# Optimization experiments

Measured on AMD Instinct MI355X. Metric: run time of the kernel, lower is better.

The kernel has to match this reference:

```python
import jax, jax.numpy as jnp
import numpy as np

BLOCKSIZE = 4096
OUT_FEATURES = 16384
IN_FEATURES = 4096
BATCH, SEQ = 4, 2048


def setup_inputs() -> dict:
    key = jax.random.key(0)
    k_x, k_w, k_a, k_b = jax.random.split(key, 4)
    x = jax.random.normal(k_x, (BATCH, SEQ, IN_FEATURES), dtype=jnp.float32)
    # quantized int8 weight stored as indices into the 256-entry codebook
    weight_q = jax.random.randint(k_w, (OUT_FEATURES, IN_FEATURES), 0, 256, dtype=jnp.int32)
    n_blocks = (OUT_FEATURES * IN_FEATURES) // BLOCKSIZE  # 16384
    absmax = jax.random.uniform(k_a, (n_blocks,), dtype=jnp.float32) + 0.5
    # bitsandbytes dynamic-map code: a sorted table of values in [-1, 1]
    code = jnp.linspace(-1.0, 1.0, 256, dtype=jnp.float32)
    bias = jax.random.normal(k_b, (OUT_FEATURES,), dtype=jnp.float32) * 0.02
    return {"x": x, "weight_q": weight_q, "absmax": absmax, "code": code, "bias": bias}


def dequantize_blockwise(weight_q, absmax, code):
    # codebook lookup then per-block absmax scaling
    flat = code[weight_q.reshape(-1)]                      # [out*in]
    flat = flat.reshape(-1, BLOCKSIZE) * absmax[:, None]   # [n_blocks, blocksize]
    return flat.reshape(weight_q.shape)                    # [out, in]


def reference(x, weight_q, absmax, code, bias):
    w = dequantize_blockwise(weight_q, absmax, code)       # [out, in] fp32
    # F.linear(x, w, bias) = x @ w.T + bias
    return jnp.einsum("bsi,oi->bso", x, w) + bias
```

## Files before the change

kernel.cpp:

```cpp
#include <hip/hip_runtime.h>
#include <hip/hip_bf16.h>
#include <stdint.h>

#define M_TOTAL 8192
#define N_TOTAL 16384
#define K_TOTAL 4096

#define BM 256
#define BN 256
#define BK 64
#define NKT (K_TOTAL / BK)

using f32x4  = __attribute__((ext_vector_type(4))) float;
using bf16x8 = __attribute__((ext_vector_type(8))) short;

#define UNROLL _Pragma("unroll")

__device__ __forceinline__ unsigned short f2bf(float f) {
    union { float f; unsigned u; } v; v.f = f;
    unsigned r = v.u + 0x7fffu + ((v.u >> 16) & 1u);
    return (unsigned short)(r >> 16);
}

__device__ __forceinline__ void gload_lds16(const void* g, void* l) {
    __builtin_amdgcn_global_load_lds(
        (const __attribute__((address_space(1))) unsigned int*)g,
        (__attribute__((address_space(3))) unsigned int*)l,
        16, 0, 0);
}

__global__ void dequant_w_kernel(const int* __restrict__ q,
                                 const float* __restrict__ am,
                                 const float* __restrict__ code,
                                 unsigned short* __restrict__ wb) {
    __shared__ float lc[256];
    if (threadIdx.x < 256) lc[threadIdx.x] = code[threadIdx.x];
    __syncthreads();
    const int total = (N_TOTAL / 4) * K_TOTAL;
    const int stride = gridDim.x * blockDim.x;
    for (int i = blockIdx.x * blockDim.x + threadIdx.x; i < total; i += stride) {
        int4 v = reinterpret_cast<const int4*>(q)[i];
        float a = am[i >> 10];
        ushort4 o;
        o.x = f2bf(lc[v.x & 255] * a);
        o.y = f2bf(lc[v.y & 255] * a);
        o.z = f2bf(lc[v.z & 255] * a);
        o.w = f2bf(lc[v.w & 255] * a);
        reinterpret_cast<ushort4*>(wb)[i] = o;
    }
}

__global__ void cvt_x_kernel(const float* __restrict__ x,
                             unsigned short* __restrict__ xb) {
    const int total = (M_TOTAL * K_TOTAL) / 4;
    const int stride = gridDim.x * blockDim.x;
    for (int i = blockIdx.x * blockDim.x + threadIdx.x; i < total; i += stride) {
        float4 v = reinterpret_cast<const float4*>(x)[i];
        ushort4 o;
        o.x = f2bf(v.x); o.y = f2bf(v.y); o.z = f2bf(v.z); o.w = f2bf(v.w);
        reinterpret_cast<ushort4*>(xb)[i] = o;
    }
}

#define LOAD_AH(DST, BUFI, MH)                                                    \
    UNROLL for (int mf = 0; mf < 4; ++mf)                                         \
        UNROLL for (int ks = 0; ks < 2; ++ks)                                     \
            DST[mf][ks] = *reinterpret_cast<const bf16x8*>(                       \
                &sA[BUFI][((MH)*128 + arow_base + mf*16)*BK +                     \
                          (((ks*4 + rslot_hi) ^ rslot_xor)*8)]);

#define LOAD_BH(DST, BUFI, NH)                                                    \
    UNROLL for (int nf = 0; nf < 2; ++nf)                                         \
        UNROLL for (int ks = 0; ks < 2; ++ks)                                     \
            DST[nf][ks] = *reinterpret_cast<const bf16x8*>(                       \
                &sB[BUFI][((NH)*128 + brow_base + nf*16)*BK +                     \
                          (((ks*4 + rslot_hi) ^ rslot_xor)*8)]);

#define MFMA_Q(MH, NH, AR, BR)                                                    \
    UNROLL for (int mf = 0; mf < 4; ++mf)                                         \
        UNROLL for (int nf = 0; nf < 2; ++nf) {                                   \
            acc[MH][mf][NH][nf] = __builtin_amdgcn_mfma_f32_16x16x32_bf16(        \
                AR[mf][0], BR[nf][0], acc[MH][mf][NH][nf], 0, 0, 0);              \
            acc[MH][mf][NH][nf] = __builtin_amdgcn_mfma_f32_16x16x32_bf16(        \
                AR[mf][1], BR[nf][1], acc[MH][mf][NH][nf], 0, 0, 0);              \
        }

#define GATE()                                                                    \
    __builtin_amdgcn_s_barrier();                                                 \
    asm volatile("s_waitcnt lgkmcnt(0)" ::: "memory");

#define TILE_BODY(BUF, NBUF, BX, BY, TS)                                          \
                                             \
    GATE();                                                                       \
    LOAD_BH(BY, BUF, 1);                                                          \
    __builtin_amdgcn_s_setprio(1); MFMA_Q(0,0,a0_r,BX);                           \
    __builtin_amdgcn_s_setprio(0);                                                \
              \
    GATE();                                                                       \
    LOAD_AH(a1_r, BUF, 1);                                                        \
    __builtin_amdgcn_s_setprio(1); MFMA_Q(0,1,a0_r,BY);                           \
    __builtin_amdgcn_s_setprio(0);                                                \
    asm volatile("s_waitcnt vmcnt(0)" ::: "memory");                              \
               \
    GATE();                                                                       \
    LOAD_AH(a0_r, NBUF, 0);                                                       \
    stA(0,0,TS,BUF); stA(0,1,TS,BUF); stA(1,0,TS,BUF); stA(1,1,TS,BUF);           \
    __builtin_amdgcn_s_setprio(1); MFMA_Q(1,1,a1_r,BY);                           \
    __builtin_amdgcn_s_setprio(0);                                                \
            \
    GATE();                                                                       \
    LOAD_BH(BY, NBUF, 0);                                                         \
    stB(0,0,TS,BUF); stB(0,1,TS,BUF); stB(1,0,TS,BUF); stB(1,1,TS,BUF);           \
    __builtin_amdgcn_s_setprio(1); MFMA_Q(1,0,a1_r,BX);                           \
    __builtin_amdgcn_s_setprio(0);

__global__ __launch_bounds__(512, 2) void gemm_pl_kernel(
        const unsigned short* __restrict__ A,
        const unsigned short* __restrict__ B,
        const float* __restrict__ bias,
        float* __restrict__ C) {
    __shared__ __align__(16) unsigned short sA[2][BM * BK];
    __shared__ __align__(16) unsigned short sB[2][BN * BK];

    const int nwg = gridDim.x;
    const int bid = blockIdx.x;
    const int wg  = (bid & 7) * (nwg >> 3) + (bid >> 3);
    const int nbn = N_TOTAL / BN;
    const int brow = (wg / nbn) * BM;
    const int bcol = (wg % nbn) * BN;

    const int tid  = threadIdx.x;
    const int wid  = tid >> 6;
    const int lane = tid & 63;
    const int wm   = wid >> 2;
    const int wn   = wid & 3;

    const int srow = wid * 8 + (lane >> 3);
    const int scol = ((lane & 7) ^ (lane >> 3)) * 8;
    const unsigned short* Asrc = A + (long long)(brow + srow) * K_TOTAL + scol;
    const unsigned short* Bsrc = B + (long long)(bcol + srow) * K_TOTAL + scol;

    auto stA = [&](int h, int j, int kt, int b) {
        gload_lds16(Asrc + (long long)(h*128 + j*64) * K_TOTAL + kt*BK,
                    &sA[b][(h*128 + j*64)*BK + wid*512]);
    };
    auto stB = [&](int h, int j, int kt, int b) {
        gload_lds16(Bsrc + (long long)(h*128 + j*64) * K_TOTAL + kt*BK,
                    &sB[b][(h*128 + j*64)*BK + wid*512]);
    };

    const int arow_base = wm * 64 + (lane & 15);
    const int brow_base = wn * 32 + (lane & 15);
    const int rslot_hi  = lane >> 4;
    const int rslot_xor = lane & 7;

    f32x4 acc[2][4][2][2];
    UNROLL for (int mh = 0; mh < 2; ++mh)
        UNROLL for (int mf = 0; mf < 4; ++mf)
            UNROLL for (int nh = 0; nh < 2; ++nh)
                UNROLL for (int nf = 0; nf < 2; ++nf)
                    acc[mh][mf][nh][nf] = (f32x4){0.f, 0.f, 0.f, 0.f};

    bf16x8 a0_r[4][2], a1_r[4][2];
    bf16x8 bx_r[2][2], by_r[2][2];

    stA(0,0,0,0); stA(0,1,0,0); stA(1,0,0,0); stA(1,1,0,0);
    stB(0,0,0,0); stB(0,1,0,0); stB(1,0,0,0); stB(1,1,0,0);
    stA(0,0,1,1); stA(0,1,1,1); stA(1,0,1,1); stA(1,1,1,1);
    stB(0,0,1,1); stB(0,1,1,1); stB(1,0,1,1); stB(1,1,1,1);
    asm volatile("s_waitcnt vmcnt(8)" ::: "memory");
    __builtin_amdgcn_s_barrier();
    LOAD_AH(a0_r, 0, 0);
    LOAD_BH(bx_r, 0, 0);

    for (int it = 0; it < NKT/2; ++it) {
        const int t0 = 2*it;
        const int s0 = (t0+2 < NKT) ? t0+2 : NKT-1;
        const int s1 = (t0+3 < NKT) ? t0+3 : NKT-1;
        TILE_BODY(0, 1, bx_r, by_r, s0)
        TILE_BODY(1, 0, by_r, bx_r, s1)
    }

    const int crow0 = (lane >> 4) * 4;
    const int ccol  = lane & 15;
    UNROLL for (int mh = 0; mh < 2; ++mh)
        UNROLL for (int mf = 0; mf < 4; ++mf) {
            const long long row0 = (long long)brow + mh*128 + wm*64 + mf*16 + crow0;
            UNROLL for (int nh = 0; nh < 2; ++nh)
                UNROLL for (int nf = 0; nf < 2; ++nf) {
                    const int col = bcol + nh*128 + wn*32 + nf*16 + ccol;
                    const float bv = bias[col];
                    UNROLL for (int r = 0; r < 4; ++r)
                        C[(row0 + r) * N_TOTAL + col] = acc[mh][mf][nh][nf][r] + bv;
                }
        }
}

extern "C" void kernel_launch(void* const* d_in, const int* in_sizes, int n_in,
                              void* d_out, int out_size, void* d_ws, size_t ws_size,
                              hipStream_t stream) {
    const float* x      = (const float*)d_in[0];
    const int*   wq     = (const int*)  d_in[1];
    const float* absmax = (const float*)d_in[2];
    const float* code   = (const float*)d_in[3];
    const float* bias   = (const float*)d_in[4];
    float* out = (float*)d_out;

    unsigned short* wb = (unsigned short*)d_ws;
    unsigned short* xb = wb + (size_t)N_TOTAL * K_TOTAL;

    dequant_w_kernel<<<2048, 256, 0, stream>>>(wq, absmax, code, wb);
    cvt_x_kernel   <<<2048, 256, 0, stream>>>(x, xb);

    dim3 grid((M_TOTAL / BM) * (N_TOTAL / BN));
    gemm_pl_kernel<<<grid, 512, 0, stream>>>(xb, wb, bias, out);
}
```

Before: 1.301 ms.

## Restructure GEMM main loop into barrier-bracketed phases with split staging

Rewrites the pipelined GEMM tile body. LDS fragments are loaded into a single A register set and two B sets, each MFMA quadrant sits between barrier open/close phases, and the global-to-LDS stores for the next tile are spread across the phases. The loop is peeled so the last two tiles skip redundant prefetches, and the LDS wait is relaxed to partial lgkmcnt counts. The aim is to cut register pressure and idle time at synchronisation points, at the cost of more barriers per tile.

```diff
diff --git a/kernel.cpp b/kernel.cpp
--- a/kernel.cpp
+++ b/kernel.cpp
@@ -62,59 +62,69 @@
     }
 }
 
-#define LOAD_AH(DST, BUFI, MH)                                                    \
+#define LOAD_A(BUFI, MH)                                                          \
     UNROLL for (int mf = 0; mf < 4; ++mf)                                         \
         UNROLL for (int ks = 0; ks < 2; ++ks)                                     \
-            DST[mf][ks] = *reinterpret_cast<const bf16x8*>(                       \
+            a_r[mf][ks] = *reinterpret_cast<const bf16x8*>(                       \
                 &sA[BUFI][((MH)*128 + arow_base + mf*16)*BK +                     \
                           (((ks*4 + rslot_hi) ^ rslot_xor)*8)]);
 
-#define LOAD_BH(DST, BUFI, NH)                                                    \
+#define LOAD_B(DST, BUFI, NH)                                                     \
     UNROLL for (int nf = 0; nf < 2; ++nf)                                         \
         UNROLL for (int ks = 0; ks < 2; ++ks)                                     \
             DST[nf][ks] = *reinterpret_cast<const bf16x8*>(                       \
                 &sB[BUFI][((NH)*128 + brow_base + nf*16)*BK +                     \
                           (((ks*4 + rslot_hi) ^ rslot_xor)*8)]);
 
-#define MFMA_Q(MH, NH, AR, BR)                                                    \
+#define MFMA_Q(MH, NH, BR)                                                        \
     UNROLL for (int mf = 0; mf < 4; ++mf)                                         \
         UNROLL for (int nf = 0; nf < 2; ++nf) {                                   \
             acc[MH][mf][NH][nf] = __builtin_amdgcn_mfma_f32_16x16x32_bf16(        \
-                AR[mf][0], BR[nf][0], acc[MH][mf][NH][nf], 0, 0, 0);              \
+                a_r[mf][0], BR[nf][0], acc[MH][mf][NH][nf], 0, 0, 0);             \
             acc[MH][mf][NH][nf] = __builtin_amdgcn_mfma_f32_16x16x32_bf16(        \
-                AR[mf][1], BR[nf][1], acc[MH][mf][NH][nf], 0, 0, 0);              \
+                a_r[mf][1], BR[nf][1], acc[MH][mf][NH][nf], 0, 0, 0);             \
         }
 
-#define GATE()                                                                    \
+#define PH_OPEN()                                                                 \
     __builtin_amdgcn_s_barrier();                                                 \
-    asm volatile("s_waitcnt lgkmcnt(0)" ::: "memory");
-
-#define TILE_BODY(BUF, NBUF, BX, BY, TS)                                          \
-                                             \
-    GATE();                                                                       \
-    LOAD_BH(BY, BUF, 1);                                                          \
-    __builtin_amdgcn_s_setprio(1); MFMA_Q(0,0,a0_r,BX);                           \
+    asm volatile("s_waitcnt lgkmcnt(0)" ::: "memory");                            \
+    __builtin_amdgcn_s_setprio(1);
+
+#define PH_CLOSE()                                                                \
     __builtin_amdgcn_s_setprio(0);                                                \
-              \
-    GATE();                                                                       \
-    LOAD_AH(a1_r, BUF, 1);                                                        \
-    __builtin_amdgcn_s_setprio(1); MFMA_Q(0,1,a0_r,BY);                           \
-    __builtin_amdgcn_s_setprio(0);                                                \
+    __builtin_amdgcn_s_barrier();
+
+#define TILE_CORE(BUF, STG, TS)                                                   \
+                                          \
+    LOAD_A(BUF, 0); LOAD_B(b0_r, BUF, 0);                                         \
+    asm volatile("s_waitcnt lgkmcnt(8)" ::: "memory");                            \
+    PH_OPEN(); MFMA_Q(0, 0, b0_r); PH_CLOSE();                                    \
+                           \
+    LOAD_B(b1_r, BUF, 1);                                                         \
+    if (STG) { stA(0,0,TS,BUF); stA(0,1,TS,BUF);                                  \
+               stB(0,0,TS,BUF); stB(0,1,TS,BUF); }                                \
+    PH_OPEN(); MFMA_Q(0, 1, b1_r); PH_CLOSE();                                    \
+                                   \
+    LOAD_A(BUF, 1);                                                               \
+    if (STG) { stB(1,0,TS,BUF); stB(1,1,TS,BUF); }                                \
+    asm volatile("s_waitcnt lgkmcnt(4)" ::: "memory");                            \
+    PH_OPEN(); MFMA_Q(1, 1, b1_r); PH_CLOSE();                                    \
+          \
+    if (STG) { stA(1,0,TS,BUF); stA(1,1,TS,BUF); }                                \
+    __builtin_amdgcn_s_barrier();                                                 \
+    __builtin_amdgcn_s_setprio(1);                                                \
+    MFMA_Q(1, 0, b0_r);                                                           \
+    __builtin_amdgcn_s_setprio(0);
+
+#define GATE8()                                                                   \
+    asm volatile("s_waitcnt vmcnt(8)" ::: "memory");                              \
+    __builtin_amdgcn_s_barrier();
+
+#define GATE0()                                                                   \
     asm volatile("s_waitcnt vmcnt(0)" ::: "memory");                              \
-               \
-    GATE();                                                                       \
-    LOAD_AH(a0_r, NBUF, 0);                                                       \
-    stA(0,0,TS,BUF); stA(0,1,TS,BUF); stA(1,0,TS,BUF); stA(1,1,TS,BUF);           \
-    __builtin_amdgcn_s_setprio(1); MFMA_Q(1,1,a1_r,BY);                           \
-    __builtin_amdgcn_s_setprio(0);                                                \
-            \
-    GATE();                                                                       \
-    LOAD_BH(BY, NBUF, 0);                                                         \
-    stB(0,0,TS,BUF); stB(0,1,TS,BUF); stB(1,0,TS,BUF); stB(1,1,TS,BUF);           \
-    __builtin_amdgcn_s_setprio(1); MFMA_Q(1,0,a1_r,BX);                           \
-    __builtin_amdgcn_s_setprio(0);
-
-__global__ __launch_bounds__(512, 2) void gemm_pl_kernel(
+    __builtin_amdgcn_s_barrier();
+
+__global__ __launch_bounds__(512, 2) void gemm_dp_kernel(
         const unsigned short* __restrict__ A,
         const unsigned short* __restrict__ B,
         const float* __restrict__ bias,
@@ -161,8 +171,8 @@
                 UNROLL for (int nf = 0; nf < 2; ++nf)
                     acc[mh][mf][nh][nf] = (f32x4){0.f, 0.f, 0.f, 0.f};
 
-    bf16x8 a0_r[4][2], a1_r[4][2];
-    bf16x8 bx_r[2][2], by_r[2][2];
+    bf16x8 a_r[4][2];
+    bf16x8 b0_r[2][2], b1_r[2][2];
 
     stA(0,0,0,0); stA(0,1,0,0); stA(1,0,0,0); stA(1,1,0,0);
     stB(0,0,0,0); stB(0,1,0,0); stB(1,0,0,0); stB(1,1,0,0);
@@ -170,16 +180,17 @@
     stB(0,0,1,1); stB(0,1,1,1); stB(1,0,1,1); stB(1,1,1,1);
     asm volatile("s_waitcnt vmcnt(8)" ::: "memory");
     __builtin_amdgcn_s_barrier();
-    LOAD_AH(a0_r, 0, 0);
-    LOAD_BH(bx_r, 0, 0);
-
-    for (int it = 0; it < NKT/2; ++it) {
+
+    for (int it = 0; it < NKT/2 - 1; ++it) {
         const int t0 = 2*it;
-        const int s0 = (t0+2 < NKT) ? t0+2 : NKT-1;
-        const int s1 = (t0+3 < NKT) ? t0+3 : NKT-1;
-        TILE_BODY(0, 1, bx_r, by_r, s0)
-        TILE_BODY(1, 0, by_r, bx_r, s1)
+        TILE_CORE(0, 1, t0 + 2)
+        GATE8();
+        TILE_CORE(1, 1, t0 + 3)
+        GATE8();
     }
+    TILE_CORE(0, 0, 0)
+    GATE0();
+    TILE_CORE(1, 0, 0)
 
     const int crow0 = (lane >> 4) * 4;
     const int ccol  = lane & 15;
@@ -213,5 +224,5 @@
     cvt_x_kernel   <<<2048, 256, 0, stream>>>(x, xb);
 
     dim3 grid((M_TOTAL / BM) * (N_TOTAL / BN));
-    gemm_pl_kernel<<<grid, 512, 0, stream>>>(xb, wb, bias, out);
-}
+    gemm_dp_kernel<<<grid, 512, 0, stream>>>(xb, wb, bias, out);
+}
```

New measurement: 1.117 ms. 14.2% less time.
